# Kernel optimization log

Hardware: AMD Instinct MI355X
Metric: run time of the kernel (lower is better)

## Reference

```python
import jax, jax.numpy as jnp
import numpy as np

D_MODEL, D_HEAD, N_HEAD = 1024, 64, 16
B, S = 8, 1024


def setup_inputs() -> dict:
    key = jax.random.key(0)
    ks = jax.random.split(key, 11)
    sc = 1.0 / np.sqrt(D_MODEL)
    inp = {
        "query": jax.random.normal(ks[0], (B, S, D_MODEL), jnp.float32),
        "key": jax.random.normal(ks[1], (B, S, D_MODEL), jnp.float32),
        "value": jax.random.normal(ks[2], (B, S, D_MODEL), jnp.float32),
        # stacked per-head Q/K projections: [H, d_model, d_head]
        "Wq": jax.random.normal(ks[3], (N_HEAD, D_MODEL, D_HEAD), jnp.float32) * sc,
        "bq": jax.random.normal(ks[4], (N_HEAD, D_HEAD), jnp.float32) * 0.01,
        "Wk": jax.random.normal(ks[5], (N_HEAD, D_MODEL, D_HEAD), jnp.float32) * sc,
        "bk": jax.random.normal(ks[6], (N_HEAD, D_HEAD), jnp.float32) * 0.01,
        # shared V projection
        "Wv": jax.random.normal(ks[7], (D_MODEL, D_HEAD), jnp.float32) * sc,
        "bv": jax.random.normal(ks[8], (D_HEAD,), jnp.float32) * 0.01,
        # output projection d_head -> d_model
        "Wo": jax.random.normal(ks[9], (D_HEAD, D_MODEL), jnp.float32) * (1.0 / np.sqrt(D_HEAD)),
        "bo": jax.random.normal(ks[10], (D_MODEL,), jnp.float32) * 0.01,
    }
    return inp


def reference(query, key, value, Wq, bq, Wk, bk, Wv, bv, Wo, bo):
    scale = D_HEAD ** -0.5
    # per-head projections, batched over heads: [B, H, S, d_head]
    Q = jnp.einsum("bsd,hdk->bhsk", query, Wq) + bq[None, :, None, :]
    K = jnp.einsum("bsd,hdk->bhsk", key, Wk) + bk[None, :, None, :]
    # shared V: [B, S, d_head]
    V = value @ Wv + bv
    # attention weights per head: [B, H, S, S]
    wei = jax.nn.softmax(jnp.einsum("bhsk,bhtk->bhst", Q, K) * scale, axis=-1)
    # head outputs averaged (shared V): [B, S, d_head]
    out = jnp.mean(jnp.einsum("bhst,btk->bhsk", wei, V), axis=1)
    return out @ Wo + bo
```

## Files before the change

### kernel.cpp

```cpp
#include <hip/hip_runtime.h>
#include <hip/hip_bf16.h>
#include <math.h>

typedef __attribute__((ext_vector_type(4))) float  f32x4;
typedef __attribute__((ext_vector_type(8))) __bf16 bf16x8;
typedef __attribute__((ext_vector_type(4))) __bf16 bf16x4;
typedef __attribute__((ext_vector_type(4))) short  s16x4;

#define SCL 0.18033688011111543f
#define MFMA16(a, b, c)   __builtin_amdgcn_mfma_f32_16x16x32_bf16((a), (b), (c), 0, 0, 0)
#define MFMA16K16(a, b, c) __builtin_amdgcn_mfma_f32_16x16x16bf16_1k((a), (b), (c), 0, 0, 0)

union B4 { bf16x4 b; s16x4 s; };

__global__ __launch_bounds__(256) void pack_qk(
    const float* __restrict__ Wq, const float* __restrict__ Wk,
    __bf16* __restrict__ WqT, __bf16* __restrict__ WkT)
{
    __shared__ __bf16 T0[64][68];
    __shared__ __bf16 T1[64][68];
    const int tid = threadIdx.x;
    const int h = blockIdx.x & 15, kt = blockIdx.x >> 4;
    const int kk = tid >> 2, cf = (tid & 3) * 16;
    const size_t base = (size_t)h * 65536 + (size_t)(kt * 64 + kk) * 64 + cf;
    #pragma unroll
    for (int j = 0; j < 4; ++j) {
        f32x4 v = *(const f32x4*)&Wq[base + 4 * j];
        f32x4 u = *(const f32x4*)&Wk[base + 4 * j];
        bf16x4 vb, ub;
        #pragma unroll
        for (int e = 0; e < 4; ++e) { vb[e] = (__bf16)v[e]; ub[e] = (__bf16)u[e]; }
        *(bf16x4*)&T0[kk][cf + 4 * j] = vb;
        *(bf16x4*)&T1[kk][cf + 4 * j] = ub;
    }
    __syncthreads();
    const int c = tid >> 2, k8 = (tid & 3) * 16;
    bf16x8 q0, q1, k0v, k1v;
    #pragma unroll
    for (int j = 0; j < 8; ++j) {
        q0[j] = T0[k8 + j][c];     q1[j] = T0[k8 + 8 + j][c];
        k0v[j] = T1[k8 + j][c];    k1v[j] = T1[k8 + 8 + j][c];
    }
    size_t dst = (size_t)(h * 64 + c) * 1024 + kt * 64 + k8;
    *(bf16x8*)&WqT[dst] = q0;  *(bf16x8*)&WqT[dst + 8] = q1;
    *(bf16x8*)&WkT[dst] = k0v; *(bf16x8*)&WkT[dst + 8] = k1v;
}

__global__ __launch_bounds__(256) void pack_misc(
    const float* __restrict__ Wv, const float* __restrict__ bv,
    const float* __restrict__ Wo,
    __bf16* __restrict__ WvT, float* __restrict__ bvP, __bf16* __restrict__ WoT)
{
    int idx = blockIdx.x * 256 + threadIdx.x;
    if (idx < 131072) {
        int n = idx >> 10, k = idx & 1023;
        WvT[idx] = (n < 64) ? (__bf16)Wv[k * 64 + n] : (__bf16)0.0f;
    }
    if (idx < 65536) {
        int n = idx >> 6, d = idx & 63;
        WoT[idx] = (__bf16)Wo[d * 1024 + n];
    }
    if (idx < 128) bvP[idx] = (idx < 64) ? bv[idx] : 0.0f;
}

__global__ __launch_bounds__(256, 2) void proj_gemm_f32(
    const float* __restrict__ A, const __bf16* __restrict__ Bt,
    const float* __restrict__ bias, __bf16* __restrict__ C)
{
    __shared__ __bf16 As[2][128][72];
    __shared__ __bf16 Bs[2][128][72];

    const int tid = threadIdx.x;
    const int lane = tid & 63, w = tid >> 6;
    const int wr = w >> 1, wc = w & 1;
    const int l15 = lane & 15, g = lane >> 4;
    const int m0 = blockIdx.x * 128, n0 = blockIdx.y * 128;
    const int arow = tid >> 4, acf = (tid & 15) * 4;
    const int brow = tid >> 3, bc8 = (tid & 7) * 8;

    f32x4 areg[8];
    bf16x8 breg[4];
    #pragma unroll
    for (int p = 0; p < 8; ++p)
        areg[p] = *(const f32x4*)&A[(size_t)(m0 + arow + 16 * p) * 1024 + acf];
    #pragma unroll
    for (int p = 0; p < 4; ++p)
        breg[p] = *(const bf16x8*)&Bt[(size_t)(n0 + brow + 32 * p) * 1024 + bc8];

    f32x4 acc[4][4] = {};
    int cur = 0;
    for (int k0 = 0; k0 < 1024; k0 += 64) {
        #pragma unroll
        for (int p = 0; p < 8; ++p) {
            bf16x4 c4;
            #pragma unroll
            for (int e = 0; e < 4; ++e) c4[e] = (__bf16)areg[p][e];
            *(bf16x4*)&As[cur][arow + 16 * p][acf] = c4;
        }
        #pragma unroll
        for (int p = 0; p < 4; ++p)
            *(bf16x8*)&Bs[cur][brow + 32 * p][bc8] = breg[p];
        if (k0 < 960) {
            #pragma unroll
            for (int p = 0; p < 8; ++p)
                areg[p] = *(const f32x4*)&A[(size_t)(m0 + arow + 16 * p) * 1024 + k0 + 64 + acf];
            #pragma unroll
            for (int p = 0; p < 4; ++p)
                breg[p] = *(const bf16x8*)&Bt[(size_t)(n0 + brow + 32 * p) * 1024 + k0 + 64 + bc8];
        }
        __syncthreads();
        __builtin_amdgcn_s_setprio(1);
        #pragma unroll
        for (int ks = 0; ks < 2; ++ks) {
            bf16x8 af[4], bfv[4];
            #pragma unroll
            for (int mi = 0; mi < 4; ++mi)
                af[mi] = *(const bf16x8*)&As[cur][64 * wr + 16 * mi + l15][32 * ks + 8 * g];
            #pragma unroll
            for (int ni = 0; ni < 4; ++ni)
                bfv[ni] = *(const bf16x8*)&Bs[cur][64 * wc + 16 * ni + l15][32 * ks + 8 * g];
            #pragma unroll
            for (int mi = 0; mi < 4; ++mi)
                #pragma unroll
                for (int ni = 0; ni < 4; ++ni)
                    acc[mi][ni] = MFMA16(af[mi], bfv[ni], acc[mi][ni]);
        }
        __builtin_amdgcn_s_setprio(0);
        cur ^= 1;
    }

    #pragma unroll
    for (int mi = 0; mi < 4; ++mi)
        #pragma unroll
        for (int ni = 0; ni < 4; ++ni) {
            int n = n0 + 64 * wc + 16 * ni + l15;
            float bn = bias[n];
            #pragma unroll
            for (int r = 0; r < 4; ++r) {
                int m = m0 + 64 * wr + 16 * mi + 4 * g + r;
                C[(size_t)m * 1024 + n] = (__bf16)(acc[mi][ni][r] + bn);
            }
        }
}

__global__ __launch_bounds__(256, 2) void proj_v(
    const float* __restrict__ A, const __bf16* __restrict__ Bt,
    const float* __restrict__ bias, __bf16* __restrict__ C)
{
    __shared__ __bf16 As[2][64][72];
    __shared__ __bf16 Bs[2][64][72];

    const int tid = threadIdx.x;
    const int lane = tid & 63, w = tid >> 6;
    const int wr = w >> 1, wc = w & 1;
    const int l15 = lane & 15, g = lane >> 4;
    const int m0 = blockIdx.x * 64;
    const int arow = tid >> 2, acf = (tid & 3) * 16;
    const int bcf = (tid & 3) * 16;

    f32x4 areg[4];
    bf16x8 breg[2];
    #pragma unroll
    for (int j = 0; j < 4; ++j)
        areg[j] = *(const f32x4*)&A[(size_t)(m0 + arow) * 1024 + acf + 4 * j];
    #pragma unroll
    for (int j = 0; j < 2; ++j)
        breg[j] = *(const bf16x8*)&Bt[(size_t)arow * 1024 + bcf + 8 * j];

    f32x4 acc[2][2] = {};
    int cur = 0;
    for (int k0 = 0; k0 < 1024; k0 += 64) {
        #pragma unroll
        for (int j = 0; j < 4; ++j) {
            bf16x4 c4;
            #pragma unroll
            for (int e = 0; e < 4; ++e) c4[e] = (__bf16)areg[j][e];
            *(bf16x4*)&As[cur][arow][acf + 4 * j] = c4;
        }
        #pragma unroll
        for (int j = 0; j < 2; ++j)
            *(bf16x8*)&Bs[cur][arow][bcf + 8 * j] = breg[j];
        if (k0 < 960) {
            #pragma unroll
            for (int j = 0; j < 4; ++j)
                areg[j] = *(const f32x4*)&A[(size_t)(m0 + arow) * 1024 + k0 + 64 + acf + 4 * j];
            #pragma unroll
            for (int j = 0; j < 2; ++j)
                breg[j] = *(const bf16x8*)&Bt[(size_t)arow * 1024 + k0 + 64 + bcf + 8 * j];
        }
        __syncthreads();
        #pragma unroll
        for (int ks = 0; ks < 2; ++ks) {
            bf16x8 af[2], bfv[2];
            #pragma unroll
            for (int mi = 0; mi < 2; ++mi)
                af[mi] = *(const bf16x8*)&As[cur][32 * wr + 16 * mi + l15][32 * ks + 8 * g];
            #pragma unroll
            for (int ni = 0; ni < 2; ++ni)
                bfv[ni] = *(const bf16x8*)&Bs[cur][32 * wc + 16 * ni + l15][32 * ks + 8 * g];
            #pragma unroll
            for (int mi = 0; mi < 2; ++mi)
                #pragma unroll
                for (int ni = 0; ni < 2; ++ni)
                    acc[mi][ni] = MFMA16(af[mi], bfv[ni], acc[mi][ni]);
        }
        __syncthreads();
        cur ^= 1;
    }

    #pragma unroll
    for (int mi = 0; mi < 2; ++mi)
        #pragma unroll
        for (int ni = 0; ni < 2; ++ni) {
            int n = 32 * wc + 16 * ni + l15;
            float bn = bias[n];
            #pragma unroll
            for (int r = 0; r < 4; ++r) {
                int m = m0 + 32 * wr + 16 * mi + 4 * g + r;
                C[(size_t)n * 8192 + m] = (__bf16)(acc[mi][ni][r] + bn);
            }
        }
}

__global__ __launch_bounds__(256, 2) void attn_kernel(
    const __bf16* __restrict__ Qb, const __bf16* __restrict__ Kb,
    const __bf16* __restrict__ Vt, __bf16* __restrict__ Oh)
{
    __shared__ __bf16 Ks[2][64][72];
    __shared__ __bf16 Vs[2][64][72];

    const int qt = blockIdx.x, bh = blockIdx.y;
    const int b = bh >> 4, h = bh & 15;
    const int tid = threadIdx.x;
    const int lane = tid & 63, w = tid >> 6;
    const int l15 = lane & 15, g = lane >> 4;
    const int s0 = b * 1024 + qt * 256;
    const int srow = tid >> 3, sc8 = (tid & 7) * 8;

    bf16x8 qf[4][2];
    #pragma unroll
    for (int mi = 0; mi < 4; ++mi)
        #pragma unroll
        for (int ks = 0; ks < 2; ++ks)
            qf[mi][ks] = *(const bf16x8*)
                &Qb[(size_t)(s0 + 64 * w + 16 * mi + l15) * 1024 + h * 64 + 32 * ks + 8 * g];

    const __bf16* Kbase = Kb + (size_t)(b * 1024) * 1024 + h * 64;
    const __bf16* Vbase = Vt + (size_t)b * 1024;

    bf16x8 kreg[2], vreg[2];
    #pragma unroll
    for (int p = 0; p < 2; ++p) {
        int r = srow + 32 * p;
        kreg[p] = *(const bf16x8*)&Kbase[(size_t)r * 1024 + sc8];
        vreg[p] = *(const bf16x8*)&Vbase[(size_t)r * 8192 + sc8];
    }

    f32x4 acc_o[4][4] = {};
    float m_run[4] = {-INFINITY, -INFINITY, -INFINITY, -INFINITY};
    float l_par[4] = {0.0f, 0.0f, 0.0f, 0.0f};

    int cur = 0;
    for (int it = 0; it < 16; ++it) {
        #pragma unroll
        for (int p = 0; p < 2; ++p) {
            int r = srow + 32 * p;
            *(bf16x8*)&Ks[cur][r][sc8] = kreg[p];
            *(bf16x8*)&Vs[cur][r][sc8] = vreg[p];
        }
        if (it < 15) {
            int t1 = (it + 1) * 64;
            #pragma unroll
            for (int p = 0; p < 2; ++p) {
                int r = srow + 32 * p;
                kreg[p] = *(const bf16x8*)&Kbase[(size_t)(t1 + r) * 1024 + sc8];
                vreg[p] = *(const bf16x8*)&Vbase[(size_t)r * 8192 + t1 + sc8];
            }
        }
        __syncthreads();

        f32x4 pacc[4][4] = {};
        __builtin_amdgcn_s_setprio(1);
        #pragma unroll
        for (int ks = 0; ks < 2; ++ks) {
            bf16x8 kf[4];
            #pragma unroll
            for (int ni = 0; ni < 4; ++ni)
                kf[ni] = *(const bf16x8*)&Ks[cur][16 * ni + l15][32 * ks + 8 * g];
            #pragma unroll
            for (int mi = 0; mi < 4; ++mi)
                #pragma unroll
                for (int ni = 0; ni < 4; ++ni)
                    pacc[mi][ni] = MFMA16(kf[ni], qf[mi][ks], pacc[mi][ni]);
        }
        __builtin_amdgcn_s_setprio(0);

        s16x4 pb[4][4];
        #pragma unroll
        for (int mi = 0; mi < 4; ++mi) {
            float tm = pacc[mi][0][0];
            #pragma unroll
            for (int ni = 0; ni < 4; ++ni)
                #pragma unroll
                for (int r = 0; r < 4; ++r)
                    tm = fmaxf(tm, pacc[mi][ni][r]);
            float ts = tm * SCL;
            ts = fmaxf(ts, __shfl_xor(ts, 16));
            ts = fmaxf(ts, __shfl_xor(ts, 32));
            if (!__all(ts <= m_run[mi] + 8.0f)) {
                float mn = fmaxf(m_run[mi], ts);
                float fsc = exp2f(m_run[mi] - mn);
                l_par[mi] *= fsc;
                #pragma unroll
                for (int nd = 0; nd < 4; ++nd) acc_o[mi][nd] *= fsc;
                m_run[mi] = mn;
            }
            float rs = 0.0f;
            #pragma unroll
            for (int ni = 0; ni < 4; ++ni) {
                B4 pk;
                #pragma unroll
                for (int r = 0; r < 4; ++r) {
                    float pv = exp2f(pacc[mi][ni][r] * SCL - m_run[mi]);
                    rs += pv;
                    pk.b[r] = (__bf16)pv;
                }
                pb[mi][ni] = pk.s;
            }
            l_par[mi] += rs;
        }

        __builtin_amdgcn_s_setprio(1);
        #pragma unroll
        for (int c = 0; c < 4; ++c) {
            s16x4 vf[4];
            #pragma unroll
            for (int nd = 0; nd < 4; ++nd) {
                B4 vv;
                vv.b = *(const bf16x4*)&Vs[cur][16 * nd + l15][16 * c + 4 * g];
                vf[nd] = vv.s;
            }
            #pragma unroll
            for (int mi = 0; mi < 4; ++mi)
                #pragma unroll
                for (int nd = 0; nd < 4; ++nd)
                    acc_o[mi][nd] = MFMA16K16(vf[nd], pb[mi][c], acc_o[mi][nd]);
        }
        __builtin_amdgcn_s_setprio(0);
        cur ^= 1;
    }

    #pragma unroll
    for (int mi = 0; mi < 4; ++mi) {
        float l = l_par[mi];
        l += __shfl_xor(l, 16);
        l += __shfl_xor(l, 32);
        float rl = 1.0f / l;
        int q = qt * 256 + 64 * w + 16 * mi + l15;
        #pragma unroll
        for (int nd = 0; nd < 4; ++nd) {
            bf16x4 ov;
            #pragma unroll
            for (int r = 0; r < 4; ++r) ov[r] = (__bf16)(acc_o[mi][nd][r] * rl);
            *(bf16x4*)&Oh[(size_t)(bh * 1024 + q) * 64 + 16 * nd + 4 * g] = ov;
        }
    }
}

__global__ __launch_bounds__(256) void mean_kernel(
    const __bf16* __restrict__ Oh, __bf16* __restrict__ Om)
{
    int idx = blockIdx.x * 256 + threadIdx.x;
    int m = idx >> 3, d8 = (idx & 7) * 8;
    int b = m >> 10, q = m & 1023;
    const __bf16* src = Oh + (size_t)(b * 16) * 65536 + (size_t)q * 64 + d8;
    float s[8] = {};
    #pragma unroll
    for (int h = 0; h < 16; ++h) {
        bf16x8 v = *(const bf16x8*)&src[(size_t)h * 65536];
        #pragma unroll
        for (int j = 0; j < 8; ++j) s[j] += (float)v[j];
    }
    bf16x8 o;
    #pragma unroll
    for (int j = 0; j < 8; ++j) o[j] = (__bf16)(s[j] * 0.0625f);
    *(bf16x8*)&Om[(size_t)m * 64 + d8] = o;
}

__global__ __launch_bounds__(256, 4) void out_gemm(
    const __bf16* __restrict__ Om, const __bf16* __restrict__ WoT,
    const float* __restrict__ bo, float* __restrict__ out)
{
    const int tid = threadIdx.x;
    const int lane = tid & 63, w = tid >> 6;
    const int wr = w >> 1, wc = w & 1;
    const int l15 = lane & 15, g = lane >> 4;
    const int m0 = blockIdx.x * 128, n0 = blockIdx.y * 128;

    f32x4 acc[4][4] = {};
    #pragma unroll
    for (int ks = 0; ks < 2; ++ks) {
        bf16x8 af[4], bfv[4];
        #pragma unroll
        for (int mi = 0; mi < 4; ++mi)
            af[mi] = *(const bf16x8*)&Om[(size_t)(m0 + 64 * wr + 16 * mi + l15) * 64 + 32 * ks + 8 * g];
        #pragma unroll
        for (int ni = 0; ni < 4; ++ni)
            bfv[ni] = *(const bf16x8*)&WoT[(size_t)(n0 + 64 * wc + 16 * ni + l15) * 64 + 32 * ks + 8 * g];
        #pragma unroll
        for (int mi = 0; mi < 4; ++mi)
            #pragma unroll
            for (int ni = 0; ni < 4; ++ni)
                acc[mi][ni] = MFMA16(af[mi], bfv[ni], acc[mi][ni]);
    }
    #pragma unroll
    for (int mi = 0; mi < 4; ++mi)
        #pragma unroll
        for (int ni = 0; ni < 4; ++ni) {
            int n = n0 + 64 * wc + 16 * ni + l15;
            float bn = bo[n];
            #pragma unroll
            for (int r = 0; r < 4; ++r) {
                int m = m0 + 64 * wr + 16 * mi + 4 * g + r;
                out[(size_t)m * 1024 + n] = acc[mi][ni][r] + bn;
            }
        }
}

extern "C" void kernel_launch(void* const* d_in, const int* in_sizes, int n_in,
                              void* d_out, int out_size, void* d_ws, size_t ws_size,
                              hipStream_t stream)
{
    const float* query = (const float*)d_in[0];
    const float* key_  = (const float*)d_in[1];
    const float* value = (const float*)d_in[2];
    const float* Wq = (const float*)d_in[3];
    const float* bq = (const float*)d_in[4];
    const float* Wk = (const float*)d_in[5];
    const float* bk = (const float*)d_in[6];
    const float* Wv = (const float*)d_in[7];
    const float* bv = (const float*)d_in[8];
    const float* Wo = (const float*)d_in[9];
    const float* bo = (const float*)d_in[10];
    float* out = (float*)d_out;

    char* p = (char*)d_ws;
    __bf16* Qbuf = (__bf16*)p; p += 8192ull * 1024 * 2;
    __bf16* Kbuf = (__bf16*)p; p += 8192ull * 1024 * 2;
    __bf16* VtB  = (__bf16*)p; p += 64ull * 8192 * 2;
    __bf16* WqT  = (__bf16*)p; p += 1024ull * 1024 * 2;
    __bf16* WkT  = (__bf16*)p; p += 1024ull * 1024 * 2;
    __bf16* WvT  = (__bf16*)p; p += 128ull * 1024 * 2;
    __bf16* WoT  = (__bf16*)p; p += 1024ull * 64 * 2;
    float*  bvP  = (float*)p;  p += 128 * 4;
    __bf16* Oh   = (__bf16*)p; p += 8ull * 16 * 1024 * 64 * 2;
    __bf16* Om   = (__bf16*)p; p += 8192ull * 64 * 2;

    pack_qk<<<256, 256, 0, stream>>>(Wq, Wk, WqT, WkT);
    pack_misc<<<512, 256, 0, stream>>>(Wv, bv, Wo, WvT, bvP, WoT);
    proj_gemm_f32<<<dim3(64, 8), 256, 0, stream>>>(query, WqT, bq, Qbuf);
    proj_gemm_f32<<<dim3(64, 8), 256, 0, stream>>>(key_,  WkT, bk, Kbuf);
    proj_v<<<128, 256, 0, stream>>>(value, WvT, bvP, VtB);
    attn_kernel<<<dim3(4, 128), 256, 0, stream>>>(Qbuf, Kbuf, VtB, Oh);
    mean_kernel<<<256, 256, 0, stream>>>(Oh, Om);
    out_gemm<<<dim3(64, 8), 256, 0, stream>>>(Om, WoT, bo, out);
}
```

Before: 164.1 us.

## Shrink attention tiles to 64 queries and 32-key blocks with 128-thread blocks

New measurement: 163.7 us. No clear change (-0.3%).

```diff
diff --git a/kernel.cpp b/kernel.cpp
--- a/kernel.cpp
+++ b/kernel.cpp
@@ -222,85 +222,83 @@
         }
 }
 
-__global__ __launch_bounds__(256, 2) void attn_kernel(
+__global__ __launch_bounds__(128, 4) void attn_kernel(
     const __bf16* __restrict__ Qb, const __bf16* __restrict__ Kb,
     const __bf16* __restrict__ Vt, __bf16* __restrict__ Oh)
 {
-    __shared__ __bf16 Ks[2][64][72];
-    __shared__ __bf16 Vs[2][64][72];
+    __shared__ __bf16 Ks[2][32][72];
+    __shared__ __bf16 Vs[2][64][40];
 
     const int qt = blockIdx.x, bh = blockIdx.y;
     const int b = bh >> 4, h = bh & 15;
     const int tid = threadIdx.x;
     const int lane = tid & 63, w = tid >> 6;
     const int l15 = lane & 15, g = lane >> 4;
-    const int s0 = b * 1024 + qt * 256;
-    const int srow = tid >> 3, sc8 = (tid & 7) * 8;
-
-    bf16x8 qf[4][2];
-    #pragma unroll
-    for (int mi = 0; mi < 4; ++mi)
+    const int s0 = b * 1024 + qt * 64;
+
+    const int krow = tid >> 2, kc = (tid & 3) * 16;
+    const int vrow = tid >> 1, vc = (tid & 1) * 16;
+
+    bf16x8 qf[2][2];
+    #pragma unroll
+    for (int mi = 0; mi < 2; ++mi)
         #pragma unroll
         for (int ks = 0; ks < 2; ++ks)
             qf[mi][ks] = *(const bf16x8*)
-                &Qb[(size_t)(s0 + 64 * w + 16 * mi + l15) * 1024 + h * 64 + 32 * ks + 8 * g];
+                &Qb[(size_t)(s0 + 32 * w + 16 * mi + l15) * 1024 + h * 64 + 32 * ks + 8 * g];
 
     const __bf16* Kbase = Kb + (size_t)(b * 1024) * 1024 + h * 64;
     const __bf16* Vbase = Vt + (size_t)b * 1024;
 
     bf16x8 kreg[2], vreg[2];
     #pragma unroll
-    for (int p = 0; p < 2; ++p) {
-        int r = srow + 32 * p;
-        kreg[p] = *(const bf16x8*)&Kbase[(size_t)r * 1024 + sc8];
-        vreg[p] = *(const bf16x8*)&Vbase[(size_t)r * 8192 + sc8];
-    }
-
-    f32x4 acc_o[4][4] = {};
-    float m_run[4] = {-INFINITY, -INFINITY, -INFINITY, -INFINITY};
-    float l_par[4] = {0.0f, 0.0f, 0.0f, 0.0f};
+    for (int j = 0; j < 2; ++j) {
+        kreg[j] = *(const bf16x8*)&Kbase[(size_t)krow * 1024 + kc + 8 * j];
+        vreg[j] = *(const bf16x8*)&Vbase[(size_t)vrow * 8192 + vc + 8 * j];
+    }
+
+    f32x4 acc_o[2][4] = {};
+    float m_run[2] = {-INFINITY, -INFINITY};
+    float l_par[2] = {0.0f, 0.0f};
 
     int cur = 0;
-    for (int it = 0; it < 16; ++it) {
-        #pragma unroll
-        for (int p = 0; p < 2; ++p) {
-            int r = srow + 32 * p;
-            *(bf16x8*)&Ks[cur][r][sc8] = kreg[p];
-            *(bf16x8*)&Vs[cur][r][sc8] = vreg[p];
-        }
-        if (it < 15) {
-            int t1 = (it + 1) * 64;
-            #pragma unroll
-            for (int p = 0; p < 2; ++p) {
-                int r = srow + 32 * p;
-                kreg[p] = *(const bf16x8*)&Kbase[(size_t)(t1 + r) * 1024 + sc8];
-                vreg[p] = *(const bf16x8*)&Vbase[(size_t)r * 8192 + t1 + sc8];
+    for (int it = 0; it < 32; ++it) {
+        *(bf16x8*)&Ks[cur][krow][kc]     = kreg[0];
+        *(bf16x8*)&Ks[cur][krow][kc + 8] = kreg[1];
+        *(bf16x8*)&Vs[cur][vrow][vc]     = vreg[0];
+        *(bf16x8*)&Vs[cur][vrow][vc + 8] = vreg[1];
+        if (it < 31) {
+            int t1 = (it + 1) * 32;
+            #pragma unroll
+            for (int j = 0; j < 2; ++j) {
+                kreg[j] = *(const bf16x8*)&Kbase[(size_t)(t1 + krow) * 1024 + kc + 8 * j];
+                vreg[j] = *(const bf16x8*)&Vbase[(size_t)vrow * 8192 + t1 + vc + 8 * j];
             }
         }
         __syncthreads();
 
-        f32x4 pacc[4][4] = {};
+        f32x4 pacc[2][2] = {};
         __builtin_amdgcn_s_setprio(1);
         #pragma unroll
         for (int ks = 0; ks < 2; ++ks) {
-            bf16x8 kf[4];
-            #pragma unroll
-            for (int ni = 0; ni < 4; ++ni)
+            bf16x8 kf[2];
+            #pragma unroll
+            for (int ni = 0; ni < 2; ++ni)
                 kf[ni] = *(const bf16x8*)&Ks[cur][16 * ni + l15][32 * ks + 8 * g];
             #pragma unroll
-            for (int mi = 0; mi < 4; ++mi)
-                #pragma unroll
-                for (int ni = 0; ni < 4; ++ni)
+            for (int mi = 0; mi < 2; ++mi)
+                #pragma unroll
+                for (int ni = 0; ni < 2; ++ni)
                     pacc[mi][ni] = MFMA16(kf[ni], qf[mi][ks], pacc[mi][ni]);
         }
         __builtin_amdgcn_s_setprio(0);
 
-        s16x4 pb[4][4];
-        #pragma unroll
-        for (int mi = 0; mi < 4; ++mi) {
+        s16x4 pb[2][2];
+        #pragma unroll
+        for (int mi = 0; mi < 2; ++mi) {
             float tm = pacc[mi][0][0];
             #pragma unroll
-            for (int ni = 0; ni < 4; ++ni)
+            for (int ni = 0; ni < 2; ++ni)
                 #pragma unroll
                 for (int r = 0; r < 4; ++r)
                     tm = fmaxf(tm, pacc[mi][ni][r]);
@@ -317,7 +315,7 @@
             }
             float rs = 0.0f;
             #pragma unroll
-            for (int ni = 0; ni < 4; ++ni) {
+            for (int ni = 0; ni < 2; ++ni) {
                 B4 pk;
                 #pragma unroll
                 for (int r = 0; r < 4; ++r) {
@@ -332,7 +330,7 @@
 
         __builtin_amdgcn_s_setprio(1);
         #pragma unroll
-        for (int c = 0; c < 4; ++c) {
+        for (int c = 0; c < 2; ++c) {
             s16x4 vf[4];
             #pragma unroll
             for (int nd = 0; nd < 4; ++nd) {
@@ -341,7 +339,7 @@
                 vf[nd] = vv.s;
             }
             #pragma unroll
-            for (int mi = 0; mi < 4; ++mi)
+            for (int mi = 0; mi < 2; ++mi)
                 #pragma unroll
                 for (int nd = 0; nd < 4; ++nd)
                     acc_o[mi][nd] = MFMA16K16(vf[nd], pb[mi][c], acc_o[mi][nd]);
@@ -351,12 +349,12 @@
     }
 
     #pragma unroll
-    for (int mi = 0; mi < 4; ++mi) {
+    for (int mi = 0; mi < 2; ++mi) {
         float l = l_par[mi];
         l += __shfl_xor(l, 16);
         l += __shfl_xor(l, 32);
         float rl = 1.0f / l;
-        int q = qt * 256 + 64 * w + 16 * mi + l15;
+        int q = qt * 64 + 32 * w + 16 * mi + l15;
         #pragma unroll
         for (int nd = 0; nd < 4; ++nd) {
             bf16x4 ov;
@@ -461,7 +459,7 @@
     proj_gemm_f32<<<dim3(64, 8), 256, 0, stream>>>(query, WqT, bq, Qbuf);
     proj_gemm_f32<<<dim3(64, 8), 256, 0, stream>>>(key_,  WkT, bk, Kbuf);
     proj_v<<<128, 256, 0, stream>>>(value, WvT, bvP, VtB);
-    attn_kernel<<<dim3(4, 128), 256, 0, stream>>>(Qbuf, Kbuf, VtB, Oh);
+    attn_kernel<<<dim3(16, 128), 128, 0, stream>>>(Qbuf, Kbuf, VtB, Oh);
     mean_kernel<<<256, 256, 0, stream>>>(Oh, Om);
     out_gemm<<<dim3(64, 8), 256, 0, stream>>>(Om, WoT, bo, out);
 }
```
